# Performance work log

Hardware: AMD Instinct MI355X
Metric: run time of the kernel (lower is better)

The kernel has to match this reference:

```python
import jax, jax.numpy as jnp
import numpy as np

N = 50000
E = 800000
D_IN = 96
D_OUT = 96


def setup_inputs() -> dict:
    key = jax.random.key(0)
    ks = jax.random.split(key, 6)
    x = jax.random.normal(ks[0], (N, D_IN), dtype=jnp.float32)
    edge_row = jax.random.randint(ks[1], (E,), 0, N, dtype=jnp.int32)
    edge_col = jax.random.randint(ks[2], (E,), 0, N, dtype=jnp.int32)
    edge_val = jax.random.uniform(ks[3], (E,), dtype=jnp.float32)
    # kaiming_uniform-ish init for weight, zeros for bias (as in reset_parameters)
    bound = float(np.sqrt(6.0 / D_IN))
    weight = jax.random.uniform(ks[4], (D_IN, D_OUT), minval=-bound, maxval=bound, dtype=jnp.float32)
    b = jnp.zeros((D_OUT,), dtype=jnp.float32)
    return {"x": x, "edge_row": edge_row, "edge_col": edge_col,
            "edge_val": edge_val, "weight": weight, "b": b}


def reference(x, edge_row, edge_col, edge_val, weight, b):
    # support = x @ W            [N, D_OUT]  (dense GEMM)
    support = x @ weight
    # spmm(adj, support): out[i] = sum_e adj_val[e] * support[col[e]] for row[e]==i
    gathered = support[edge_col] * edge_val[:, None]          # [E, D_OUT]
    out = jax.ops.segment_sum(gathered, edge_row, num_segments=x.shape[0])
    return out + b
```

## Files before the change

kernel.cpp:

```cpp
#include <hip/hip_runtime.h>
#include <hip/hip_fp16.h>

#define D 96
#define SLOTS 48
#define NBUCKET 256
#define BCAP 5120
#define RPBMAX 200
#define CHUNK 2048
#define BSTRIDE 16

typedef __attribute__((ext_vector_type(8))) short short8;
typedef __attribute__((ext_vector_type(4))) float f32x4;

__device__ inline unsigned short f32_to_bf16_rne(float f) {
    unsigned int u = __float_as_uint(f);
    unsigned int r = u + 0x7FFFu + ((u >> 16) & 1u);
    return (unsigned short)(r >> 16);
}

__global__ __launch_bounds__(256) void gemm_mfma(const float* __restrict__ x,
                                                 const float* __restrict__ w,
                                                 __half* __restrict__ support,
                                                 int n) {
    __shared__ unsigned short Wl[96 * 98];
    __shared__ unsigned short Xl[64 * 100];
    const int tid = threadIdx.x;

    {
        const float4* w4 = (const float4*)w;
        #pragma unroll
        for (int it = 0; it < 9; it++) {
            int i4 = tid + it * 256;
            if (i4 < 2304) {
                int r = i4 / 24, c = i4 - (i4 / 24) * 24;
                float4 v = w4[i4];
                unsigned int p0 = (unsigned int)f32_to_bf16_rne(v.x) |
                                  ((unsigned int)f32_to_bf16_rne(v.y) << 16);
                unsigned int p1 = (unsigned int)f32_to_bf16_rne(v.z) |
                                  ((unsigned int)f32_to_bf16_rne(v.w) << 16);
                unsigned int* dst = (unsigned int*)&Wl[r * 98 + c * 4];
                dst[0] = p0; dst[1] = p1;
            }
        }
    }

    const int row0 = blockIdx.x * 64;
    int nrows = n - row0;
    if (nrows > 64) nrows = 64;
    {
        const float4* x4 = (const float4*)(x + (size_t)row0 * D);
        const int lim = nrows * 24;
        #pragma unroll
        for (int it = 0; it < 6; it++) {
            int i4 = tid + it * 256;
            if (i4 < lim) {
                int r = i4 / 24, c = i4 - (i4 / 24) * 24;
                float4 v = x4[i4];
                unsigned int p0 = (unsigned int)f32_to_bf16_rne(v.x) |
                                  ((unsigned int)f32_to_bf16_rne(v.y) << 16);
                unsigned int p1 = (unsigned int)f32_to_bf16_rne(v.z) |
                                  ((unsigned int)f32_to_bf16_rne(v.w) << 16);
                unsigned int* dst = (unsigned int*)&Xl[r * 100 + c * 4];
                dst[0] = p0; dst[1] = p1;
            }
        }
    }
    __syncthreads();

    const int lane = tid & 63;
    const int wave = tid >> 6;
    const int m0 = (blockIdx.x * 4 + wave) * 16;
    if (m0 >= n) return;

    const int quad = lane >> 4;
    const int col = lane & 15;

    short8 bf[18];
    #pragma unroll
    for (int f = 0; f < 18; f++) {
        int ct = f / 3, kc = f - ct * 3;
        const unsigned short* base = &Wl[(kc * 32 + quad * 8) * 98 + ct * 16 + col];
        #pragma unroll
        for (int j = 0; j < 8; j++) bf[f][j] = (short)base[j * 98];
    }

    f32x4 acc[6];
    #pragma unroll
    for (int ct = 0; ct < 6; ct++) acc[ct] = (f32x4){0.f, 0.f, 0.f, 0.f};

    const int lrow = (wave * 16 + col);
    #pragma unroll
    for (int kc = 0; kc < 3; kc++) {
        const unsigned short* ax = &Xl[lrow * 100 + kc * 32 + quad * 8];
        short8 a;
        #pragma unroll
        for (int j = 0; j < 8; j++) a[j] = (short)ax[j];
        #pragma unroll
        for (int ct = 0; ct < 6; ct++)
            acc[ct] = __builtin_amdgcn_mfma_f32_16x16x32_bf16(a, bf[ct * 3 + kc], acc[ct], 0, 0, 0);
    }

    const int rbase = m0 + quad * 4;
    #pragma unroll
    for (int ct = 0; ct < 6; ct++) {
        #pragma unroll
        for (int j = 0; j < 4; j++) {
            support[(size_t)(rbase + j) * D + ct * 16 + col] = __float2half(acc[ct][j]);
        }
    }
}

__global__ __launch_bounds__(256) void partition_edges(const int* __restrict__ erow,
                                                       const int* __restrict__ ecol,
                                                       const float* __restrict__ eval_,
                                                       unsigned int* __restrict__ bcnt,
                                                       uint2* __restrict__ recs,
                                                       int E, int RPB) {
    __shared__ unsigned int lcnt[NBUCKET];
    __shared__ unsigned int l2cnt[NBUCKET];
    __shared__ unsigned int scan[NBUCKET];
    __shared__ unsigned int loffs[NBUCKET];
    __shared__ unsigned int gbase[NBUCKET];
    __shared__ uint2 rec[CHUNK];

    const int tid = threadIdx.x;
    const int c0 = blockIdx.x * CHUNK;
    const int tot = min(CHUNK, E - c0);

    lcnt[tid] = 0; l2cnt[tid] = 0;
    __syncthreads();

    #pragma unroll
    for (int k = 0; k < CHUNK / 256; k++) {
        int i = k * 256 + tid;
        if (i < tot) {
            int r = erow[c0 + i];
            atomicAdd(&lcnt[r / RPB], 1u);
        }
    }
    __syncthreads();

    scan[tid] = lcnt[tid];
    __syncthreads();
    for (int d = 1; d < NBUCKET; d <<= 1) {
        unsigned int v = scan[tid];
        unsigned int add = (tid >= d) ? scan[tid - d] : 0u;
        __syncthreads();
        scan[tid] = v + add;
        __syncthreads();
    }
    loffs[tid] = scan[tid] - lcnt[tid];
    __syncthreads();

    #pragma unroll
    for (int k = 0; k < CHUNK / 256; k++) {
        int i = k * 256 + tid;
        if (i < tot) {
            int r = erow[c0 + i];
            int bk = r / RPB;
            int rl = r - bk * RPB;
            unsigned int pk = (unsigned int)(unsigned short)ecol[c0 + i] |
                              ((unsigned int)__half_as_ushort(__float2half_rn(eval_[c0 + i])) << 16);
            unsigned int s = atomicAdd(&l2cnt[bk], 1u);
            rec[loffs[bk] + s] = make_uint2(pk, ((unsigned int)bk << 8) | (unsigned int)rl);
        }
    }
    __syncthreads();

    gbase[tid] = atomicAdd(&bcnt[tid * BSTRIDE], lcnt[tid]);
    __syncthreads();

    for (int i = tid; i < tot; i += 256) {
        uint2 rr = rec[i];
        unsigned int bk = (rr.y >> 8) & 0xFFu;
        unsigned int dst = gbase[bk] + ((unsigned int)i - loffs[bk]);
        if (dst < BCAP) recs[(size_t)bk * BCAP + dst] = rr;
    }
}

__global__ __launch_bounds__(768) void bucket_accumulate(const unsigned int* __restrict__ bcnt,
                                                         const uint2* __restrict__ recs,
                                                         const __half* __restrict__ support,
                                                         const float* __restrict__ bias,
                                                         float* __restrict__ out,
                                                         int N, int RPB) {
    __shared__ unsigned int cnt_l[RPBMAX];
    __shared__ unsigned int slots_l[RPBMAX * SLOTS];
    const int tid = threadIdx.x;
    const int bkt = blockIdx.x;

    for (int i = tid; i < RPBMAX; i += 768) cnt_l[i] = 0;
    __syncthreads();

    unsigned int m = bcnt[bkt * BSTRIDE];
    if (m > BCAP) m = BCAP;
    const uint2* br = recs + (size_t)bkt * BCAP;
    for (unsigned int i = tid; i < m; i += 768) {
        uint2 rr = br[i];
        unsigned int rl = rr.y & 0xFFu;
        unsigned int s = atomicAdd(&cnt_l[rl], 1u);
        if (s < SLOTS) slots_l[rl * SLOTS + s] = rr.x;
    }
    __syncthreads();

    const int rg = tid / 12;
    const int c  = tid - rg * 12;
    const float4* sup16 = (const float4*)support;
    const float4 bA = ((const float4*)bias)[c * 2];
    const float4 bB = ((const float4*)bias)[c * 2 + 1];

    for (int rl = rg; rl < RPB; rl += 64) {
        int r = bkt * RPB + rl;
        if (r >= N) break;
        int deg = (int)cnt_l[rl];
        if (deg > SLOTS) deg = SLOTS;
        const unsigned int* sl = &slots_l[rl * SLOTS];

        float4 accA = bA;
        float4 accB = bB;

        int i = 0;
        for (; i + 4 <= deg; i += 4) {
            unsigned int u0 = sl[i + 0];
            unsigned int u1 = sl[i + 1];
            unsigned int u2 = sl[i + 2];
            unsigned int u3 = sl[i + 3];
            float4 g0 = sup16[(size_t)(u0 & 0xFFFFu) * 12 + c];
            float4 g1 = sup16[(size_t)(u1 & 0xFFFFu) * 12 + c];
            float4 g2 = sup16[(size_t)(u2 & 0xFFFFu) * 12 + c];
            float4 g3 = sup16[(size_t)(u3 & 0xFFFFu) * 12 + c];
            float v0 = __half2float(__ushort_as_half((unsigned short)(u0 >> 16)));
            float v1 = __half2float(__ushort_as_half((unsigned short)(u1 >> 16)));
            float v2 = __half2float(__ushort_as_half((unsigned short)(u2 >> 16)));
            float v3 = __half2float(__ushort_as_half((unsigned short)(u3 >> 16)));

            const __half2* h;
            h = (const __half2*)&g0;
            { float2 f0 = __half22float2(h[0]), f1 = __half22float2(h[1]),
                     f2 = __half22float2(h[2]), f3 = __half22float2(h[3]);
              accA.x += v0 * f0.x; accA.y += v0 * f0.y; accA.z += v0 * f1.x; accA.w += v0 * f1.y;
              accB.x += v0 * f2.x; accB.y += v0 * f2.y; accB.z += v0 * f3.x; accB.w += v0 * f3.y; }
            h = (const __half2*)&g1;
            { float2 f0 = __half22float2(h[0]), f1 = __half22float2(h[1]),
                     f2 = __half22float2(h[2]), f3 = __half22float2(h[3]);
              accA.x += v1 * f0.x; accA.y += v1 * f0.y; accA.z += v1 * f1.x; accA.w += v1 * f1.y;
              accB.x += v1 * f2.x; accB.y += v1 * f2.y; accB.z += v1 * f3.x; accB.w += v1 * f3.y; }
            h = (const __half2*)&g2;
            { float2 f0 = __half22float2(h[0]), f1 = __half22float2(h[1]),
                     f2 = __half22float2(h[2]), f3 = __half22float2(h[3]);
              accA.x += v2 * f0.x; accA.y += v2 * f0.y; accA.z += v2 * f1.x; accA.w += v2 * f1.y;
              accB.x += v2 * f2.x; accB.y += v2 * f2.y; accB.z += v2 * f3.x; accB.w += v2 * f3.y; }
            h = (const __half2*)&g3;
            { float2 f0 = __half22float2(h[0]), f1 = __half22float2(h[1]),
                     f2 = __half22float2(h[2]), f3 = __half22float2(h[3]);
              accA.x += v3 * f0.x; accA.y += v3 * f0.y; accA.z += v3 * f1.x; accA.w += v3 * f1.y;
              accB.x += v3 * f2.x; accB.y += v3 * f2.y; accB.z += v3 * f3.x; accB.w += v3 * f3.y; }
        }
        for (; i < deg; i++) {
            unsigned int u = sl[i];
            float4 g = sup16[(size_t)(u & 0xFFFFu) * 12 + c];
            float v = __half2float(__ushort_as_half((unsigned short)(u >> 16)));
            const __half2* h = (const __half2*)&g;
            float2 f0 = __half22float2(h[0]), f1 = __half22float2(h[1]),
                   f2 = __half22float2(h[2]), f3 = __half22float2(h[3]);
            accA.x += v * f0.x; accA.y += v * f0.y; accA.z += v * f1.x; accA.w += v * f1.y;
            accB.x += v * f2.x; accB.y += v * f2.y; accB.z += v * f3.x; accB.w += v * f3.y;
        }

        float* o = out + (size_t)r * D + c * 8;
        f32x4 sA = {accA.x, accA.y, accA.z, accA.w};
        f32x4 sB = {accB.x, accB.y, accB.z, accB.w};
        __builtin_nontemporal_store(sA, (f32x4*)o);
        __builtin_nontemporal_store(sB, (f32x4*)(o + 4));
    }
}

extern "C" void kernel_launch(void* const* d_in, const int* in_sizes, int n_in,
                              void* d_out, int out_size, void* d_ws, size_t ws_size,
                              hipStream_t stream) {
    const float* x     = (const float*)d_in[0];
    const int*   erow  = (const int*)d_in[1];
    const int*   ecol  = (const int*)d_in[2];
    const float* eval_ = (const float*)d_in[3];
    const float* w     = (const float*)d_in[4];
    const float* bias  = (const float*)d_in[5];
    float* out = (float*)d_out;

    const int n = in_sizes[0] / D;
    const int E = in_sizes[1];

    const size_t supBytes  = (size_t)n * D * sizeof(__half);
    const size_t bcntBytes = (size_t)NBUCKET * BSTRIDE * sizeof(unsigned int);

    __half*       support = (__half*)d_ws;
    unsigned int* bcnt    = (unsigned int*)((char*)d_ws + supBytes);
    uint2*        recs    = (uint2*)((char*)d_ws + supBytes + bcntBytes);

    const int RPB = (n + NBUCKET - 1) / NBUCKET;

    hipMemsetAsync(bcnt, 0, bcntBytes, stream);

    gemm_mfma<<<(n + 63) / 64, 256, 0, stream>>>(x, w, support, n);
    partition_edges<<<(E + CHUNK - 1) / CHUNK, 256, 0, stream>>>(erow, ecol, eval_,
                                                                 bcnt, recs, E, RPB);
    bucket_accumulate<<<NBUCKET, 768, 0, stream>>>(bcnt, recs, support, bias, out, n, RPB);
}
```

Measured before the change: 130.5 us.

## Merge GEMM and edge partition into one launch with interleaved block roles

Fuses the independent dense GEMM and edge-partitioning kernels into a single launch. Every third block, up to the partition block count, does partitioning and the rest do GEMM tiles. Their shared memory is overlaid through a union. This removes one kernel launch and the serialization gap between the two independent stages so they run concurrently. The cost is a larger union LDS footprint for GEMM blocks, which may reduce occupancy.

```diff
diff --git a/kernel.cpp b/kernel.cpp
--- a/kernel.cpp
+++ b/kernel.cpp
@@ -18,13 +18,83 @@
     return (unsigned short)(r >> 16);
 }
 
-__global__ __launch_bounds__(256) void gemm_mfma(const float* __restrict__ x,
-                                                 const float* __restrict__ w,
-                                                 __half* __restrict__ support,
-                                                 int n) {
-    __shared__ unsigned short Wl[96 * 98];
-    __shared__ unsigned short Xl[64 * 100];
+__global__ __launch_bounds__(256) void gemm_and_partition(const float* __restrict__ x,
+                                                          const float* __restrict__ w,
+                                                          __half* __restrict__ support,
+                                                          const int* __restrict__ erow,
+                                                          const int* __restrict__ ecol,
+                                                          const float* __restrict__ eval_,
+                                                          unsigned int* __restrict__ bcnt,
+                                                          uint2* __restrict__ recs,
+                                                          int n, int E, int PB, int RPB) {
+    __shared__ union U {
+        struct { unsigned short Wl[96 * 98]; unsigned short Xl[64 * 100]; } g;
+        struct { unsigned int lcnt[NBUCKET], l2cnt[NBUCKET], scan[NBUCKET],
+                              loffs[NBUCKET], gbase[NBUCKET]; uint2 rec[CHUNK]; } p;
+    } sh;
+
+    const int bid = blockIdx.x;
+    const int q = bid / 3;
+    const bool is_part = ((bid - q * 3) == 2) && (q < PB);
     const int tid = threadIdx.x;
+
+    if (is_part) {
+        const int c0 = q * CHUNK;
+        const int tot = min(CHUNK, E - c0);
+
+        sh.p.lcnt[tid] = 0; sh.p.l2cnt[tid] = 0;
+        __syncthreads();
+
+        #pragma unroll
+        for (int k = 0; k < CHUNK / 256; k++) {
+            int i = k * 256 + tid;
+            if (i < tot) {
+                int r = erow[c0 + i];
+                atomicAdd(&sh.p.lcnt[r / RPB], 1u);
+            }
+        }
+        __syncthreads();
+
+        sh.p.scan[tid] = sh.p.lcnt[tid];
+        __syncthreads();
+        for (int d = 1; d < NBUCKET; d <<= 1) {
+            unsigned int v = sh.p.scan[tid];
+            unsigned int add = (tid >= d) ? sh.p.scan[tid - d] : 0u;
+            __syncthreads();
+            sh.p.scan[tid] = v + add;
+            __syncthreads();
+        }
+        sh.p.loffs[tid] = sh.p.scan[tid] - sh.p.lcnt[tid];
+        __syncthreads();
+
+        #pragma unroll
+        for (int k = 0; k < CHUNK / 256; k++) {
+            int i = k * 256 + tid;
+            if (i < tot) {
+                int r = erow[c0 + i];
+                int bk = r / RPB;
+                int rl = r - bk * RPB;
+                unsigned int pk = (unsigned int)(unsigned short)ecol[c0 + i] |
+                                  ((unsigned int)__half_as_ushort(__float2half_rn(eval_[c0 + i])) << 16);
+                unsigned int s = atomicAdd(&sh.p.l2cnt[bk], 1u);
+                sh.p.rec[sh.p.loffs[bk] + s] = make_uint2(pk, ((unsigned int)bk << 8) | (unsigned int)rl);
+            }
+        }
+        __syncthreads();
+
+        sh.p.gbase[tid] = atomicAdd(&bcnt[tid * BSTRIDE], sh.p.lcnt[tid]);
+        __syncthreads();
+
+        for (int i = tid; i < tot; i += 256) {
+            uint2 rr = sh.p.rec[i];
+            unsigned int bk = (rr.y >> 8) & 0xFFu;
+            unsigned int dst = sh.p.gbase[bk] + ((unsigned int)i - sh.p.loffs[bk]);
+            if (dst < BCAP) recs[(size_t)bk * BCAP + dst] = rr;
+        }
+        return;
+    }
+
+    const int g = bid - min(q, PB);
 
     {
         const float4* w4 = (const float4*)w;
@@ -38,13 +108,13 @@
                                   ((unsigned int)f32_to_bf16_rne(v.y) << 16);
                 unsigned int p1 = (unsigned int)f32_to_bf16_rne(v.z) |
                                   ((unsigned int)f32_to_bf16_rne(v.w) << 16);
-                unsigned int* dst = (unsigned int*)&Wl[r * 98 + c * 4];
+                unsigned int* dst = (unsigned int*)&sh.g.Wl[r * 98 + c * 4];
                 dst[0] = p0; dst[1] = p1;
             }
         }
     }
 
-    const int row0 = blockIdx.x * 64;
+    const int row0 = g * 64;
     int nrows = n - row0;
     if (nrows > 64) nrows = 64;
     {
@@ -60,7 +130,7 @@
                                   ((unsigned int)f32_to_bf16_rne(v.y) << 16);
                 unsigned int p1 = (unsigned int)f32_to_bf16_rne(v.z) |
                                   ((unsigned int)f32_to_bf16_rne(v.w) << 16);
-                unsigned int* dst = (unsigned int*)&Xl[r * 100 + c * 4];
+                unsigned int* dst = (unsigned int*)&sh.g.Xl[r * 100 + c * 4];
                 dst[0] = p0; dst[1] = p1;
             }
         }
@@ -69,7 +139,7 @@
 
     const int lane = tid & 63;
     const int wave = tid >> 6;
-    const int m0 = (blockIdx.x * 4 + wave) * 16;
+    const int m0 = (g * 4 + wave) * 16;
     if (m0 >= n) return;
 
     const int quad = lane >> 4;
@@ -79,7 +149,7 @@
     #pragma unroll
     for (int f = 0; f < 18; f++) {
         int ct = f / 3, kc = f - ct * 3;
-        const unsigned short* base = &Wl[(kc * 32 + quad * 8) * 98 + ct * 16 + col];
+        const unsigned short* base = &sh.g.Wl[(kc * 32 + quad * 8) * 98 + ct * 16 + col];
         #pragma unroll
         for (int j = 0; j < 8; j++) bf[f][j] = (short)base[j * 98];
     }
@@ -91,7 +161,7 @@
     const int lrow = (wave * 16 + col);
     #pragma unroll
     for (int kc = 0; kc < 3; kc++) {
-        const unsigned short* ax = &Xl[lrow * 100 + kc * 32 + quad * 8];
+        const unsigned short* ax = &sh.g.Xl[lrow * 100 + kc * 32 + quad * 8];
         short8 a;
         #pragma unroll
         for (int j = 0; j < 8; j++) a[j] = (short)ax[j];
@@ -107,74 +177,6 @@
         for (int j = 0; j < 4; j++) {
             support[(size_t)(rbase + j) * D + ct * 16 + col] = __float2half(acc[ct][j]);
         }
-    }
-}
-
-__global__ __launch_bounds__(256) void partition_edges(const int* __restrict__ erow,
-                                                       const int* __restrict__ ecol,
-                                                       const float* __restrict__ eval_,
-                                                       unsigned int* __restrict__ bcnt,
-                                                       uint2* __restrict__ recs,
-                                                       int E, int RPB) {
-    __shared__ unsigned int lcnt[NBUCKET];
-    __shared__ unsigned int l2cnt[NBUCKET];
-    __shared__ unsigned int scan[NBUCKET];
-    __shared__ unsigned int loffs[NBUCKET];
-    __shared__ unsigned int gbase[NBUCKET];
-    __shared__ uint2 rec[CHUNK];
-
-    const int tid = threadIdx.x;
-    const int c0 = blockIdx.x * CHUNK;
-    const int tot = min(CHUNK, E - c0);
-
-    lcnt[tid] = 0; l2cnt[tid] = 0;
-    __syncthreads();
-
-    #pragma unroll
-    for (int k = 0; k < CHUNK / 256; k++) {
-        int i = k * 256 + tid;
-        if (i < tot) {
-            int r = erow[c0 + i];
-            atomicAdd(&lcnt[r / RPB], 1u);
-        }
-    }
-    __syncthreads();
-
-    scan[tid] = lcnt[tid];
-    __syncthreads();
-    for (int d = 1; d < NBUCKET; d <<= 1) {
-        unsigned int v = scan[tid];
-        unsigned int add = (tid >= d) ? scan[tid - d] : 0u;
-        __syncthreads();
-        scan[tid] = v + add;
-        __syncthreads();
-    }
-    loffs[tid] = scan[tid] - lcnt[tid];
-    __syncthreads();
-
-    #pragma unroll
-    for (int k = 0; k < CHUNK / 256; k++) {
-        int i = k * 256 + tid;
-        if (i < tot) {
-            int r = erow[c0 + i];
-            int bk = r / RPB;
-            int rl = r - bk * RPB;
-            unsigned int pk = (unsigned int)(unsigned short)ecol[c0 + i] |
-                              ((unsigned int)__half_as_ushort(__float2half_rn(eval_[c0 + i])) << 16);
-            unsigned int s = atomicAdd(&l2cnt[bk], 1u);
-            rec[loffs[bk] + s] = make_uint2(pk, ((unsigned int)bk << 8) | (unsigned int)rl);
-        }
-    }
-    __syncthreads();
-
-    gbase[tid] = atomicAdd(&bcnt[tid * BSTRIDE], lcnt[tid]);
-    __syncthreads();
-
-    for (int i = tid; i < tot; i += 256) {
-        uint2 rr = rec[i];
-        unsigned int bk = (rr.y >> 8) & 0xFFu;
-        unsigned int dst = gbase[bk] + ((unsigned int)i - loffs[bk]);
-        if (dst < BCAP) recs[(size_t)bk * BCAP + dst] = rr;
     }
 }
 
@@ -300,8 +302,9 @@
 
     hipMemsetAsync(bcnt, 0, bcntBytes, stream);
 
-    gemm_mfma<<<(n + 63) / 64, 256, 0, stream>>>(x, w, support, n);
-    partition_edges<<<(E + CHUNK - 1) / CHUNK, 256, 0, stream>>>(erow, ecol, eval_,
-                                                                 bcnt, recs, E, RPB);
+    const int GB = (n + 63) / 64;
+    const int PB = (E + CHUNK - 1) / CHUNK;
+    gemm_and_partition<<<GB + PB, 256, 0, stream>>>(x, w, support, erow, ecol, eval_,
+                                                    bcnt, recs, n, E, PB, RPB);
     bucket_accumulate<<<NBUCKET, 768, 0, stream>>>(bcnt, recs, support, bias, out, n, RPB);
 }
```

Result: faster. 123.1 us, median of 2 (-5.6%).
